# Kernel optimization log

Hardware: AMD Instinct MI355X
Metric: run time of the kernel (lower is better)

## Reference

```python
import jax, jax.numpy as jnp
import numpy as np
from jax import lax

HIDDEN = 2048
INTER = 4096          # mamba_expand * hidden_size
HEADS = 64
HEAD_DIM = 64         # HEADS * HEAD_DIM == INTER
STATE = 64
GROUPS = 1
KCONV = 4
CONV_DIM = INTER + 2 * GROUPS * STATE   # 4224
PROJ = INTER + CONV_DIM + HEADS          # 8384
SSM_IN_MULT = 1.0
Z_MULT, X_MULT, B_MULT, C_MULT, DT_MULT = 1.0, 1.0, 1.0, 1.0, 1.0
EPS = 1e-6


def setup_inputs() -> dict:
    key = jax.random.key(0)
    ks = jax.random.split(key, 4)
    B, L = 1, 2048
    return {
        "hidden_states": jax.random.normal(ks[0], (B, L, HIDDEN), jnp.float32),
        "in_proj_w": jax.random.normal(ks[1], (PROJ, HIDDEN), jnp.float32) / np.sqrt(HIDDEN),
        "conv_w": jax.random.normal(ks[2], (CONV_DIM, KCONV), jnp.float32) / np.sqrt(KCONV),
        "conv_b": jnp.zeros((CONV_DIM,), jnp.float32),
        "dt_bias": jnp.ones((HEADS,), jnp.float32),
        "A_log": jnp.log(jnp.arange(1, HEADS + 1, dtype=jnp.float32)),
        "D": jnp.ones((HEADS,), jnp.float32),
        "norm_weight": jnp.ones((INTER,), jnp.float32),
        "out_proj_w": jax.random.normal(ks[3], (HIDDEN, INTER), jnp.float32) / np.sqrt(INTER),
    }


def reference(hidden_states, in_proj_w, conv_w, conv_b, dt_bias, A_log, D,
              norm_weight, out_proj_w):
    Bsz, L, _ = hidden_states.shape
    gns = GROUPS * STATE

    # ----- in_proj + per-split multipliers -----
    proj = (hidden_states * SSM_IN_MULT) @ in_proj_w.T          # [B,L,PROJ]
    gate = proj[..., :INTER] * Z_MULT                           # z
    hBC = proj[..., INTER:INTER + CONV_DIM]
    dt = proj[..., INTER + CONV_DIM:] * DT_MULT                 # [B,L,H]
    hBC = jnp.concatenate(
        [hBC[..., :INTER] * X_MULT,
         hBC[..., INTER:INTER + gns] * B_MULT,
         hBC[..., INTER + gns:] * C_MULT], axis=-1)

    # ----- causal depthwise conv1d (left pad K-1, truncate to L) + SiLU -----
    padded = jnp.pad(hBC, ((0, 0), (KCONV - 1, 0), (0, 0)))
    conv = conv_b
    for k in range(KCONV):
        conv = conv + padded[:, k:k + L, :] * conv_w[:, k]
    hBC = jax.nn.silu(conv)

    x = hBC[..., :INTER].reshape(Bsz, L, HEADS, HEAD_DIM)       # [B,L,H,P]
    Bm = hBC[..., INTER:INTER + gns].reshape(Bsz, L, GROUPS, STATE)
    Cm = hBC[..., INTER + gns:].reshape(Bsz, L, GROUPS, STATE)
    hpg = HEADS // GROUPS
    B_h = jnp.repeat(Bm, hpg, axis=2)                           # [B,L,H,N]
    C_h = jnp.repeat(Cm, hpg, axis=2)

    # ----- selective SSM recurrence -----
    dt = jax.nn.softplus(dt + dt_bias)                          # [B,L,H] (>0; clamp(0,inf) no-op)
    A = -jnp.exp(A_log)                                         # [H]
    dA = jnp.exp(dt * A)                                        # [B,L,H]
    dtx = dt[..., None] * x                                     # [B,L,H,P]

    def step(s, inp):
        dA_t, dtx_t, B_t, C_t = inp                             # [B,H], [B,H,P], [B,H,N], [B,H,N]
        s = dA_t[..., None, None] * s + dtx_t[..., None] * B_t[:, :, None, :]
        y_t = jnp.einsum('bhpn,bhn->bhp', s, C_t)
        return s, y_t

    tm = lambda a: jnp.moveaxis(a, 1, 0)  # time-major
    s0 = jnp.zeros((Bsz, HEADS, HEAD_DIM, STATE), jnp.float32)
    _, ys = lax.scan(step, s0, (tm(dA), tm(dtx), tm(B_h), tm(C_h)))
    y = jnp.moveaxis(ys, 0, 1) + D[None, None, :, None] * x     # [B,L,H,P]
    y = y.reshape(Bsz, L, INTER)

    # ----- gated RMSNorm (norm before gate) -----
    yg = y.reshape(Bsz, L, GROUPS, INTER // GROUPS)
    var = jnp.mean(yg * yg, axis=-1, keepdims=True)
    yg = yg * lax.rsqrt(var + EPS) * norm_weight.reshape(GROUPS, INTER // GROUPS)
    y = yg.reshape(Bsz, L, INTER) * jax.nn.silu(gate)

    return y @ out_proj_w.T                                     # [B,L,HIDDEN]
```

## Files before the change

kernel.cpp:

```cpp
#include <hip/hip_runtime.h>
#include <hip/hip_bf16.h>
#include <cstdint>
#include <cstddef>

#define SEQLEN   2048
#define HIDDEN   2048
#define INTER    4096
#define NHEADS   64
#define NSTATE   64
#define CONVD    4224
#define LDPROJ   8448
#define NCHUNK   32
#define CHUNK    64

typedef __attribute__((ext_vector_type(8))) short bf16x8_t;
typedef __attribute__((ext_vector_type(4))) float f32x4_t;

__device__ __forceinline__ void cp16(void* lds, const void* g) {
    __builtin_amdgcn_global_load_lds(
        (const __attribute__((address_space(1))) unsigned int*)g,
        (__attribute__((address_space(3))) unsigned int*)lds, 16, 0, 0);
}

__global__ void k_split(const float* __restrict__ in, unsigned short* __restrict__ hi,
                        unsigned short* __restrict__ lo, long nvalid, long ntotal) {
    long i = (long)blockIdx.x * 256 + threadIdx.x;
    if (i >= ntotal) return;
    float x = (i < nvalid) ? in[i] : 0.0f;
    __hip_bfloat16 h = __float2bfloat16(x);
    float hf = __bfloat162float(h);
    __hip_bfloat16 l = __float2bfloat16(x - hf);
    hi[i] = *reinterpret_cast<unsigned short*>(&h);
    lo[i] = *reinterpret_cast<unsigned short*>(&l);
}

__global__ __launch_bounds__(256, 2)
void k_gemm_split(const unsigned short* __restrict__ Ah, const unsigned short* __restrict__ Al,
                  const unsigned short* __restrict__ Bh, const unsigned short* __restrict__ Bl,
                  float* __restrict__ C, int K, int ldc) {
    __shared__ unsigned short sA[2][128 * 32];
    __shared__ unsigned short sB[2][128 * 32];

    const int tid  = threadIdx.x;
    const int lane = tid & 63;
    const int w    = tid >> 6;
    const int wm   = w >> 1, wn = w & 1;
    const long bm  = (long)blockIdx.y * 128;
    const long bn  = (long)blockIdx.x * 128;

    f32x4_t acc[4][4];
#pragma unroll
    for (int i = 0; i < 4; ++i)
#pragma unroll
        for (int j = 0; j < 4; ++j) acc[i][j] = (f32x4_t){0.f, 0.f, 0.f, 0.f};

    const int l4 = lane >> 2;
    const int c8 = (lane & 3) << 3;
    const int ar = lane & 15;
    const int kq = (lane >> 4) << 3;

    for (int k0 = 0; k0 < K; k0 += 32) {
#pragma unroll
        for (int j = 0; j < 2; ++j) {
            const int chunk = j * 4 + w;
            const int r     = chunk * 16 + l4;
            const long gA   = (bm + r) * (long)K + k0 + c8;
            const long gB   = (bn + r) * (long)K + k0 + c8;
            const int lbase = chunk * 512;
            cp16(&sA[0][lbase], Ah + gA);
            cp16(&sA[1][lbase], Al + gA);
            cp16(&sB[0][lbase], Bh + gB);
            cp16(&sB[1][lbase], Bl + gB);
        }
        __syncthreads();

        bf16x8_t fah[4], fal[4], fbh[4], fbl[4];
#pragma unroll
        for (int mi = 0; mi < 4; ++mi) {
            int row = wm * 64 + mi * 16 + ar;
            fah[mi] = *(const bf16x8_t*)&sA[0][row * 32 + kq];
            fal[mi] = *(const bf16x8_t*)&sA[1][row * 32 + kq];
        }
#pragma unroll
        for (int ni = 0; ni < 4; ++ni) {
            int row = wn * 64 + ni * 16 + ar;
            fbh[ni] = *(const bf16x8_t*)&sB[0][row * 32 + kq];
            fbl[ni] = *(const bf16x8_t*)&sB[1][row * 32 + kq];
        }
#pragma unroll
        for (int mi = 0; mi < 4; ++mi)
#pragma unroll
            for (int ni = 0; ni < 4; ++ni) {
                acc[mi][ni] = __builtin_amdgcn_mfma_f32_16x16x32_bf16(fah[mi], fbh[ni], acc[mi][ni], 0, 0, 0);
                acc[mi][ni] = __builtin_amdgcn_mfma_f32_16x16x32_bf16(fah[mi], fbl[ni], acc[mi][ni], 0, 0, 0);
                acc[mi][ni] = __builtin_amdgcn_mfma_f32_16x16x32_bf16(fal[mi], fbh[ni], acc[mi][ni], 0, 0, 0);
            }
        __syncthreads();
    }

    const int col = lane & 15;
    const int rq  = (lane >> 4) << 2;
#pragma unroll
    for (int mi = 0; mi < 4; ++mi)
#pragma unroll
        for (int ni = 0; ni < 4; ++ni) {
            long mb = bm + wm * 64 + mi * 16 + rq;
            long nb = bn + wn * 64 + ni * 16 + col;
#pragma unroll
            for (int r = 0; r < 4; ++r) C[(mb + r) * (long)ldc + nb] = acc[mi][ni][r];
        }
}

__global__ void k_conv(const float* __restrict__ proj, const float* __restrict__ cw,
                       const float* __restrict__ cb, float* __restrict__ xbc) {
    int c = blockIdx.x * 256 + threadIdx.x;
    int t = blockIdx.y;
    if (c >= CONVD) return;
    float acc = cb[c];
#pragma unroll
    for (int k = 0; k < 4; ++k) {
        int tt = t - 3 + k;
        if (tt >= 0) acc += proj[(size_t)tt * LDPROJ + INTER + c] * cw[c * 4 + k];
    }
    float s = acc / (1.f + expf(-acc));
    xbc[(size_t)t * CONVD + c] = s;
}

__global__ __launch_bounds__(256)
void k_cum(const float* __restrict__ proj, const float* __restrict__ dtb,
           float* __restrict__ dt, float* __restrict__ cd) {
    const int tid  = threadIdx.x;
    const int lane = tid & 63;
    const int wid  = blockIdx.x * 4 + (tid >> 6);
    const int c    = wid >> 6;
    const int h    = wid & 63;
    const int t    = c * CHUNK + lane;
    float raw = proj[(size_t)t * LDPROJ + 8320 + h] + dtb[h];
    float sp  = (raw > 20.f) ? raw : log1pf(expf(raw));
    float x = sp;
#pragma unroll
    for (int off = 1; off < 64; off <<= 1) {
        float v = __shfl_up(x, off, 64);
        if (lane >= off) x += v;
    }
    dt[t * 64 + h] = sp;
    cd[t * 64 + h] = x;
}

__global__ __launch_bounds__(256, 2)
void k_ssdA(const float* __restrict__ xbc, const float* __restrict__ dt,
            const float* __restrict__ cd, const float* __restrict__ alog,
            const float* __restrict__ Dp, float* __restrict__ y,
            float* __restrict__ M) {
    __shared__ float Xs[64][68];
    __shared__ float Bs[64][68];
    __shared__ float Cs[64][68];
    __shared__ float dts[64], cds[64], wts[64];
    float (*Gs)[68] = Cs;

    const int c = blockIdx.x, h = blockIdx.y;
    const int tid = threadIdx.x;
    const int tr = tid >> 4, tc = tid & 15;
    const int t0 = c * CHUNK;
    const float A = -__expf(alog[h]);

    for (int i = tid; i < 4096; i += 256) {
        int t = i >> 6, j = i & 63;
        size_t base = (size_t)(t0 + t) * CONVD;
        Xs[t][j] = xbc[base + h * 64 + j];
        Bs[t][j] = xbc[base + INTER + j];
        Cs[t][j] = xbc[base + INTER + 64 + j];
    }
    if (tid < 64) {
        dts[tid] = dt[(t0 + tid) * 64 + h];
        cds[tid] = cd[(t0 + tid) * 64 + h];
    }
    __syncthreads();
    if (tid < 64) wts[tid] = __expf(A * (cds[63] - cds[tid])) * dts[tid];

    float g[4][4];
#pragma unroll
    for (int i = 0; i < 4; ++i)
#pragma unroll
        for (int j = 0; j < 4; ++j) g[i][j] = 0.f;
    for (int n = 0; n < 64; n += 4) {
        float4 cv[4], bv[4];
#pragma unroll
        for (int i = 0; i < 4; ++i) cv[i] = *(const float4*)&Cs[tr * 4 + i][n];
#pragma unroll
        for (int j = 0; j < 4; ++j) bv[j] = *(const float4*)&Bs[tc * 4 + j][n];
#pragma unroll
        for (int i = 0; i < 4; ++i)
#pragma unroll
            for (int j = 0; j < 4; ++j)
                g[i][j] += cv[i].x * bv[j].x + cv[i].y * bv[j].y +
                           cv[i].z * bv[j].z + cv[i].w * bv[j].w;
    }
    __syncthreads();
#pragma unroll
    for (int i = 0; i < 4; ++i) {
        int t = tr * 4 + i;
#pragma unroll
        for (int j = 0; j < 4; ++j) {
            int tau = tc * 4 + j;
            float v = (tau <= t) ? g[i][j] * __expf(A * (cds[t] - cds[tau])) * dts[tau] : 0.f;
            Gs[t][tau] = v;
        }
    }
    __syncthreads();

    float accY[4][4], accM[4][4];
#pragma unroll
    for (int i = 0; i < 4; ++i)
#pragma unroll
        for (int j = 0; j < 4; ++j) { accY[i][j] = 0.f; accM[i][j] = 0.f; }

    for (int tau = 0; tau < 64; tau += 4) {
        float4 gv[4], xv[4];
#pragma unroll
        for (int i = 0; i < 4; ++i) gv[i] = *(const float4*)&Gs[tr * 4 + i][tau];
#pragma unroll
        for (int k = 0; k < 4; ++k) xv[k] = *(const float4*)&Xs[tau + k][tc * 4];
#pragma unroll
        for (int i = 0; i < 4; ++i) {
            accY[i][0] += gv[i].x * xv[0].x + gv[i].y * xv[1].x + gv[i].z * xv[2].x + gv[i].w * xv[3].x;
            accY[i][1] += gv[i].x * xv[0].y + gv[i].y * xv[1].y + gv[i].z * xv[2].y + gv[i].w * xv[3].y;
            accY[i][2] += gv[i].x * xv[0].z + gv[i].y * xv[1].z + gv[i].z * xv[2].z + gv[i].w * xv[3].z;
            accY[i][3] += gv[i].x * xv[0].w + gv[i].y * xv[1].w + gv[i].z * xv[2].w + gv[i].w * xv[3].w;
        }
#pragma unroll
        for (int k = 0; k < 4; ++k) {
            float w = wts[tau + k];
            float4 bv = *(const float4*)&Bs[tau + k][tr * 4];
            float4 xk = xv[k];
            float wb0 = w * bv.x, wb1 = w * bv.y, wb2 = w * bv.z, wb3 = w * bv.w;
            accM[0][0] += wb0 * xk.x; accM[0][1] += wb0 * xk.y; accM[0][2] += wb0 * xk.z; accM[0][3] += wb0 * xk.w;
            accM[1][0] += wb1 * xk.x; accM[1][1] += wb1 * xk.y; accM[1][2] += wb1 * xk.z; accM[1][3] += wb1 * xk.w;
            accM[2][0] += wb2 * xk.x; accM[2][1] += wb2 * xk.y; accM[2][2] += wb2 * xk.z; accM[2][3] += wb2 * xk.w;
            accM[3][0] += wb3 * xk.x; accM[3][1] += wb3 * xk.y; accM[3][2] += wb3 * xk.z; accM[3][3] += wb3 * xk.w;
        }
    }

    const float Dv = Dp[h];
#pragma unroll
    for (int i = 0; i < 4; ++i) {
        int t = tr * 4 + i;
        float4 o;
        o.x = accY[i][0] + Dv * Xs[t][tc * 4 + 0];
        o.y = accY[i][1] + Dv * Xs[t][tc * 4 + 1];
        o.z = accY[i][2] + Dv * Xs[t][tc * 4 + 2];
        o.w = accY[i][3] + Dv * Xs[t][tc * 4 + 3];
        *(float4*)&y[(size_t)(t0 + t) * INTER + h * 64 + tc * 4] = o;
    }
    size_t mbase = ((size_t)(c * 64 + h)) << 12;
#pragma unroll
    for (int i = 0; i < 4; ++i) {
        float4 o = { accM[i][0], accM[i][1], accM[i][2], accM[i][3] };
        *(float4*)&M[mbase + (size_t)(tr * 4 + i) * 64 + tc * 4] = o;
    }
}

__global__ __launch_bounds__(256)
void k_state(const float* __restrict__ M, const float* __restrict__ cd,
             const float* __restrict__ alog, float* __restrict__ Sprev) {
    const int g  = blockIdx.x * 256 + threadIdx.x;
    const int h  = g >> 12;
    const int np = g & 4095;
    const float A = -__expf(alog[h]);
    float s = 0.f;
#pragma unroll 1
    for (int c = 0; c < NCHUNK; ++c) {
        size_t idx = (((size_t)(c * 64 + h)) << 12) + np;
        Sprev[idx] = s;
        float decay = __expf(A * cd[((c * CHUNK + 63) * 64) + h]);
        s = decay * s + M[idx];
    }
}

__global__ __launch_bounds__(256, 2)
void k_ssdC(const float* __restrict__ xbc, const float* __restrict__ cd,
            const float* __restrict__ alog, const float* __restrict__ Sprev,
            float* __restrict__ y) {
    __shared__ float Ss[64][68];
    __shared__ float Cs[64][68];
    __shared__ float cds[64];
    const int c = blockIdx.x, h = blockIdx.y;
    const int tid = threadIdx.x;
    const int tr = tid >> 4, tc = tid & 15;
    const int t0 = c * CHUNK;
    const float A = -__expf(alog[h]);

    size_t sbase = ((size_t)(c * 64 + h)) << 12;
    for (int i = tid; i < 4096; i += 256) {
        int n = i >> 6, p = i & 63;
        Ss[n][p] = Sprev[sbase + i];
        Cs[n][p] = xbc[(size_t)(t0 + n) * CONVD + INTER + 64 + p];
    }
    if (tid < 64) cds[tid] = cd[(t0 + tid) * 64 + h];
    __syncthreads();

    float acc[4][4];
#pragma unroll
    for (int i = 0; i < 4; ++i)
#pragma unroll
        for (int j = 0; j < 4; ++j) acc[i][j] = 0.f;

    for (int n = 0; n < 64; n += 4) {
        float4 cv[4], sv[4];
#pragma unroll
        for (int i = 0; i < 4; ++i) cv[i] = *(const float4*)&Cs[tr * 4 + i][n];
#pragma unroll
        for (int k = 0; k < 4; ++k) sv[k] = *(const float4*)&Ss[n + k][tc * 4];
#pragma unroll
        for (int i = 0; i < 4; ++i) {
            acc[i][0] += cv[i].x * sv[0].x + cv[i].y * sv[1].x + cv[i].z * sv[2].x + cv[i].w * sv[3].x;
            acc[i][1] += cv[i].x * sv[0].y + cv[i].y * sv[1].y + cv[i].z * sv[2].y + cv[i].w * sv[3].y;
            acc[i][2] += cv[i].x * sv[0].z + cv[i].y * sv[1].z + cv[i].z * sv[2].z + cv[i].w * sv[3].z;
            acc[i][3] += cv[i].x * sv[0].w + cv[i].y * sv[1].w + cv[i].z * sv[2].w + cv[i].w * sv[3].w;
        }
    }

#pragma unroll
    for (int i = 0; i < 4; ++i) {
        int t = tr * 4 + i;
        float sc = __expf(A * cds[t]);
        size_t yi = (size_t)(t0 + t) * INTER + h * 64 + tc * 4;
        float4 cur = *(const float4*)&y[yi];
        cur.x += sc * acc[i][0];
        cur.y += sc * acc[i][1];
        cur.z += sc * acc[i][2];
        cur.w += sc * acc[i][3];
        *(float4*)&y[yi] = cur;
    }
}

__global__ __launch_bounds__(256)
void k_norm(const float* __restrict__ y, const float* __restrict__ proj,
            const float* __restrict__ nw, unsigned short* __restrict__ ygh,
            unsigned short* __restrict__ ygl) {
    __shared__ float red[4];
    const int t = blockIdx.x, tid = threadIdx.x;
    float sum = 0.f;
    for (int i = tid; i < INTER; i += 256) {
        float v = y[(size_t)t * INTER + i];
        sum += v * v;
    }
#pragma unroll
    for (int off = 32; off >= 1; off >>= 1) sum += __shfl_xor(sum, off, 64);
    if ((tid & 63) == 0) red[tid >> 6] = sum;
    __syncthreads();
    float var = (red[0] + red[1] + red[2] + red[3]) * (1.f / INTER);
    float rs  = rsqrtf(var + 1e-6f);
    for (int i = tid; i < INTER; i += 256) {
        float v = y[(size_t)t * INTER + i] * rs * nw[i];
        float g = proj[(size_t)t * LDPROJ + i];
        float o = v * (g / (1.f + expf(-g)));
        __hip_bfloat16 hh = __float2bfloat16(o);
        float hf = __bfloat162float(hh);
        __hip_bfloat16 ll = __float2bfloat16(o - hf);
        ygh[(size_t)t * INTER + i] = *reinterpret_cast<unsigned short*>(&hh);
        ygl[(size_t)t * INTER + i] = *reinterpret_cast<unsigned short*>(&ll);
    }
}

#define OFF_HSHI  ((size_t)0)
#define OFF_HSLO  ((size_t)8388608)
#define OFF_YGH   ((size_t)0)
#define OFF_W1HI  ((size_t)16777216)
#define OFF_W1LO  ((size_t)(16777216 + 34603008))
#define OFF_M     ((size_t)16777216)
#define OFF_SPREV ((size_t)50331648)
#define OFF_W2HI  ((size_t)16777216)
#define OFF_W2LO  ((size_t)33554432)
#define OFF_PROJ  ((size_t)85983232)
#define OFF_XBC   ((size_t)155189248)
#define OFF_DT    ((size_t)189792256)
#define OFF_CD    ((size_t)190316544)
#define OFF_Y     ((size_t)190840832)
#define OFF_YGL   ((size_t)224395264)

extern "C" void kernel_launch(void* const* d_in, const int* in_sizes, int n_in,
                              void* d_out, int out_size, void* d_ws, size_t ws_size,
                              hipStream_t stream) {
    (void)in_sizes; (void)n_in; (void)out_size; (void)ws_size;
    const float* hs   = (const float*)d_in[0];
    const float* w1   = (const float*)d_in[1];
    const float* cw   = (const float*)d_in[2];
    const float* cb   = (const float*)d_in[3];
    const float* dtb  = (const float*)d_in[4];
    const float* alog = (const float*)d_in[5];
    const float* Dp   = (const float*)d_in[6];
    const float* nw   = (const float*)d_in[7];
    const float* w2   = (const float*)d_in[8];
    float* out = (float*)d_out;
    char* ws = (char*)d_ws;

    unsigned short* hs_hi = (unsigned short*)(ws + OFF_HSHI);
    unsigned short* hs_lo = (unsigned short*)(ws + OFF_HSLO);
    unsigned short* w1_hi = (unsigned short*)(ws + OFF_W1HI);
    unsigned short* w1_lo = (unsigned short*)(ws + OFF_W1LO);
    unsigned short* w2_hi = (unsigned short*)(ws + OFF_W2HI);
    unsigned short* w2_lo = (unsigned short*)(ws + OFF_W2LO);
    unsigned short* ygh   = (unsigned short*)(ws + OFF_YGH);
    unsigned short* ygl   = (unsigned short*)(ws + OFF_YGL);
    float* proj  = (float*)(ws + OFF_PROJ);
    float* xbc   = (float*)(ws + OFF_XBC);
    float* dtv   = (float*)(ws + OFF_DT);
    float* cdv   = (float*)(ws + OFF_CD);
    float* y     = (float*)(ws + OFF_Y);
    float* M     = (float*)(ws + OFF_M);
    float* Sprev = (float*)(ws + OFF_SPREV);

    k_split<<<16384, 256, 0, stream>>>(hs, hs_hi, hs_lo, 4194304L, 4194304L);
    k_split<<<67584, 256, 0, stream>>>(w1, w1_hi, w1_lo, 17170432L, 17301504L);

    k_gemm_split<<<dim3(66, 16), 256, 0, stream>>>(hs_hi, hs_lo, w1_hi, w1_lo, proj, HIDDEN, LDPROJ);

    k_conv<<<dim3(17, SEQLEN), 256, 0, stream>>>(proj, cw, cb, xbc);
    k_cum<<<512, 256, 0, stream>>>(proj, dtb, dtv, cdv);

    k_ssdA<<<dim3(NCHUNK, NHEADS), 256, 0, stream>>>(xbc, dtv, cdv, alog, Dp, y, M);
    k_state<<<1024, 256, 0, stream>>>(M, cdv, alog, Sprev);
    k_ssdC<<<dim3(NCHUNK, NHEADS), 256, 0, stream>>>(xbc, cdv, alog, Sprev, y);

    k_norm<<<SEQLEN, 256, 0, stream>>>(y, proj, nw, ygh, ygl);

    k_split<<<32768, 256, 0, stream>>>(w2, w2_hi, w2_lo, 8388608L, 8388608L);

    k_gemm_split<<<dim3(16, 16), 256, 0, stream>>>(ygh, ygl, w2_hi, w2_lo, out, INTER, HIDDEN);
}
```

Before: 770.7 us.

## Use single bf16 pass for in_proj columns except dt, add block swizzle

The in_proj GEMM now runs the three-term hi/lo split (bf16x3) only for output columns at or past 8192, the dt and padding block. All other columns (z, x, B, C) use one hi*hi bf16 MFMA and skip loading the lo tiles. The lo split of w1 is computed only for those tail rows. The change also adds a strip-wise block index swizzle for L2 reuse and switches the LDS layout to contiguous per-lane 16-byte fragments. The risk is lower precision for the gate and conv inputs, which may exceed the tolerance.

Measured after the change: 818.3 us. +6.2%, slower.

```diff
diff --git a/kernel.cpp b/kernel.cpp
--- a/kernel.cpp
+++ b/kernel.cpp
@@ -34,10 +34,31 @@
     lo[i] = *reinterpret_cast<unsigned short*>(&l);
 }
 
+__global__ void k_split_hi(const float* __restrict__ in, unsigned short* __restrict__ hi,
+                           long nvalid, long ntotal) {
+    long i = (long)blockIdx.x * 256 + threadIdx.x;
+    if (i >= ntotal) return;
+    float x = (i < nvalid) ? in[i] : 0.0f;
+    __hip_bfloat16 h = __float2bfloat16(x);
+    hi[i] = *reinterpret_cast<unsigned short*>(&h);
+}
+
+__global__ void k_split_lo(const float* __restrict__ in, unsigned short* __restrict__ lo,
+                           long nvalid, long ntotal) {
+    long i = (long)blockIdx.x * 256 + threadIdx.x;
+    if (i >= ntotal) return;
+    float x = (i < nvalid) ? in[i] : 0.0f;
+    __hip_bfloat16 h = __float2bfloat16(x);
+    float hf = __bfloat162float(h);
+    __hip_bfloat16 l = __float2bfloat16(x - hf);
+    lo[i] = *reinterpret_cast<unsigned short*>(&l);
+}
+
 __global__ __launch_bounds__(256, 2)
 void k_gemm_split(const unsigned short* __restrict__ Ah, const unsigned short* __restrict__ Al,
                   const unsigned short* __restrict__ Bh, const unsigned short* __restrict__ Bl,
-                  float* __restrict__ C, int K, int ldc) {
+                  float* __restrict__ C, int K, int ldc,
+                  int mb_count, int strip_w, int split_col) {
     __shared__ unsigned short sA[2][128 * 32];
     __shared__ unsigned short sB[2][128 * 32];
 
@@ -45,8 +66,15 @@
     const int lane = tid & 63;
     const int w    = tid >> 6;
     const int wm   = w >> 1, wn = w & 1;
-    const long bm  = (long)blockIdx.y * 128;
-    const long bn  = (long)blockIdx.x * 128;
+
+    const int span  = mb_count * strip_w;
+    const int strip = blockIdx.x / span;
+    const int within = blockIdx.x % span;
+    const int mblk = within % mb_count;
+    const int nblk = strip * strip_w + within / mb_count;
+    const long bm  = (long)mblk * 128;
+    const long bn  = (long)nblk * 128;
+    const bool do_lo = (bn >= (long)split_col);
 
     f32x4_t acc[4][4];
 #pragma unroll
@@ -54,47 +82,57 @@
 #pragma unroll
         for (int j = 0; j < 4; ++j) acc[i][j] = (f32x4_t){0.f, 0.f, 0.f, 0.f};
 
-    const int l4 = lane >> 2;
-    const int c8 = (lane & 3) << 3;
-    const int ar = lane & 15;
-    const int kq = (lane >> 4) << 3;
+    const int srow = lane & 15;
+    const int c8   = (lane >> 4) << 3;
 
     for (int k0 = 0; k0 < K; k0 += 32) {
 #pragma unroll
         for (int j = 0; j < 2; ++j) {
             const int chunk = j * 4 + w;
-            const int r     = chunk * 16 + l4;
+            const int r     = chunk * 16 + srow;
             const long gA   = (bm + r) * (long)K + k0 + c8;
             const long gB   = (bn + r) * (long)K + k0 + c8;
             const int lbase = chunk * 512;
             cp16(&sA[0][lbase], Ah + gA);
-            cp16(&sA[1][lbase], Al + gA);
             cp16(&sB[0][lbase], Bh + gB);
-            cp16(&sB[1][lbase], Bl + gB);
+            if (do_lo) {
+                cp16(&sA[1][lbase], Al + gA);
+                cp16(&sB[1][lbase], Bl + gB);
+            }
         }
         __syncthreads();
 
-        bf16x8_t fah[4], fal[4], fbh[4], fbl[4];
-#pragma unroll
-        for (int mi = 0; mi < 4; ++mi) {
-            int row = wm * 64 + mi * 16 + ar;
-            fah[mi] = *(const bf16x8_t*)&sA[0][row * 32 + kq];
-            fal[mi] = *(const bf16x8_t*)&sA[1][row * 32 + kq];
-        }
-#pragma unroll
-        for (int ni = 0; ni < 4; ++ni) {
-            int row = wn * 64 + ni * 16 + ar;
-            fbh[ni] = *(const bf16x8_t*)&sB[0][row * 32 + kq];
-            fbl[ni] = *(const bf16x8_t*)&sB[1][row * 32 + kq];
-        }
+        bf16x8_t fah[4], fbh[4];
 #pragma unroll
         for (int mi = 0; mi < 4; ++mi)
-#pragma unroll
-            for (int ni = 0; ni < 4; ++ni) {
-                acc[mi][ni] = __builtin_amdgcn_mfma_f32_16x16x32_bf16(fah[mi], fbh[ni], acc[mi][ni], 0, 0, 0);
-                acc[mi][ni] = __builtin_amdgcn_mfma_f32_16x16x32_bf16(fah[mi], fbl[ni], acc[mi][ni], 0, 0, 0);
-                acc[mi][ni] = __builtin_amdgcn_mfma_f32_16x16x32_bf16(fal[mi], fbh[ni], acc[mi][ni], 0, 0, 0);
-            }
+            fah[mi] = *(const bf16x8_t*)&sA[0][(wm * 4 + mi) * 512 + lane * 8];
+#pragma unroll
+        for (int ni = 0; ni < 4; ++ni)
+            fbh[ni] = *(const bf16x8_t*)&sB[0][(wn * 4 + ni) * 512 + lane * 8];
+
+        if (do_lo) {
+            bf16x8_t fal[4], fbl[4];
+#pragma unroll
+            for (int mi = 0; mi < 4; ++mi)
+                fal[mi] = *(const bf16x8_t*)&sA[1][(wm * 4 + mi) * 512 + lane * 8];
+#pragma unroll
+            for (int ni = 0; ni < 4; ++ni)
+                fbl[ni] = *(const bf16x8_t*)&sB[1][(wn * 4 + ni) * 512 + lane * 8];
+#pragma unroll
+            for (int mi = 0; mi < 4; ++mi)
+#pragma unroll
+                for (int ni = 0; ni < 4; ++ni) {
+                    acc[mi][ni] = __builtin_amdgcn_mfma_f32_16x16x32_bf16(fah[mi], fbh[ni], acc[mi][ni], 0, 0, 0);
+                    acc[mi][ni] = __builtin_amdgcn_mfma_f32_16x16x32_bf16(fah[mi], fbl[ni], acc[mi][ni], 0, 0, 0);
+                    acc[mi][ni] = __builtin_amdgcn_mfma_f32_16x16x32_bf16(fal[mi], fbh[ni], acc[mi][ni], 0, 0, 0);
+                }
+        } else {
+#pragma unroll
+            for (int mi = 0; mi < 4; ++mi)
+#pragma unroll
+                for (int ni = 0; ni < 4; ++ni)
+                    acc[mi][ni] = __builtin_amdgcn_mfma_f32_16x16x32_bf16(fah[mi], fbh[ni], acc[mi][ni], 0, 0, 0);
+        }
         __syncthreads();
     }
 
@@ -104,10 +142,10 @@
     for (int mi = 0; mi < 4; ++mi)
 #pragma unroll
         for (int ni = 0; ni < 4; ++ni) {
-            long mb = bm + wm * 64 + mi * 16 + rq;
-            long nb = bn + wn * 64 + ni * 16 + col;
-#pragma unroll
-            for (int r = 0; r < 4; ++r) C[(mb + r) * (long)ldc + nb] = acc[mi][ni][r];
+            long mb_ = bm + wm * 64 + mi * 16 + rq;
+            long nb_ = bn + wn * 64 + ni * 16 + col;
+#pragma unroll
+            for (int r = 0; r < 4; ++r) C[(mb_ + r) * (long)ldc + nb_] = acc[mi][ni][r];
         }
 }
 
@@ -230,10 +268,10 @@
         }
 #pragma unroll
         for (int k = 0; k < 4; ++k) {
-            float w = wts[tau + k];
+            float wv = wts[tau + k];
             float4 bv = *(const float4*)&Bs[tau + k][tr * 4];
             float4 xk = xv[k];
-            float wb0 = w * bv.x, wb1 = w * bv.y, wb2 = w * bv.z, wb3 = w * bv.w;
+            float wb0 = wv * bv.x, wb1 = wv * bv.y, wb2 = wv * bv.z, wb3 = wv * bv.w;
             accM[0][0] += wb0 * xk.x; accM[0][1] += wb0 * xk.y; accM[0][2] += wb0 * xk.z; accM[0][3] += wb0 * xk.w;
             accM[1][0] += wb1 * xk.x; accM[1][1] += wb1 * xk.y; accM[1][2] += wb1 * xk.z; accM[1][3] += wb1 * xk.w;
             accM[2][0] += wb2 * xk.x; accM[2][1] += wb2 * xk.y; accM[2][2] += wb2 * xk.z; accM[2][3] += wb2 * xk.w;
@@ -412,9 +450,12 @@
     float* Sprev = (float*)(ws + OFF_SPREV);
 
     k_split<<<16384, 256, 0, stream>>>(hs, hs_hi, hs_lo, 4194304L, 4194304L);
-    k_split<<<67584, 256, 0, stream>>>(w1, w1_hi, w1_lo, 17170432L, 17301504L);
-
-    k_gemm_split<<<dim3(66, 16), 256, 0, stream>>>(hs_hi, hs_lo, w1_hi, w1_lo, proj, HIDDEN, LDPROJ);
+    k_split_hi<<<67584, 256, 0, stream>>>(w1, w1_hi, 17170432L, 17301504L);
+    k_split_lo<<<2048, 256, 0, stream>>>(w1 + (size_t)8192 * 2048, w1_lo, 393216L, 524288L);
+
+    const unsigned short* w1_lo_base = w1_lo - (size_t)8192 * 2048;
+    k_gemm_split<<<1056, 256, 0, stream>>>(hs_hi, hs_lo, w1_hi, w1_lo_base, proj,
+                                           HIDDEN, LDPROJ, 16, 6, 8192);
 
     k_conv<<<dim3(17, SEQLEN), 256, 0, stream>>>(proj, cw, cb, xbc);
     k_cum<<<512, 256, 0, stream>>>(proj, dtb, dtv, cdv);
@@ -427,5 +468,6 @@
 
     k_split<<<32768, 256, 0, stream>>>(w2, w2_hi, w2_lo, 8388608L, 8388608L);
 
-    k_gemm_split<<<dim3(16, 16), 256, 0, stream>>>(ygh, ygl, w2_hi, w2_lo, out, INTER, HIDDEN);
-}
+    k_gemm_split<<<256, 256, 0, stream>>>(ygh, ygl, w2_hi, w2_lo, out,
+                                          INTER, HIDDEN, 16, 4, 0);
+}
```
